# Kernel optimization log

Measured on AMD Instinct MI355X. Metric: run time of the kernel, lower is better.

The kernel has to match this reference:

```python
import jax, jax.numpy as jnp
import numpy as np

B, N, INPUT_DIM = 32, 4096, 256
BASE = 32           # base_feat_dim
A = 5               # n_aggs
E = 48              # per_agg_dim
H = 2               # num_agg_heads
HD = E // H         # head dim = 24
AGG_DIM = BASE * A  # 160
HIDDEN = 512
EXTRA_IN = INPUT_DIM - AGG_DIM   # 96
EXTRA_OUT = HIDDEN - E * A       # 272


def setup_inputs() -> dict:
    key = jax.random.key(0)
    ks = jax.random.split(key, 10)
    s = 0.05
    return {
        "x": jax.random.normal(ks[0], (B, N, INPUT_DIM), dtype=jnp.float32),
        # 5 per-group Linear(base_feat_dim -> 48), stacked: [A, E, BASE]
        "agg_W": jax.random.normal(ks[1], (A, E, BASE), dtype=jnp.float32) * s,
        "agg_b": jax.random.normal(ks[2], (A, E), dtype=jnp.float32) * s,
        # MultiheadAttention packed in-projection [3E, E] and bias [3E]
        "in_proj_w": jax.random.normal(ks[3], (3 * E, E), dtype=jnp.float32) * s,
        "in_proj_b": jax.random.normal(ks[4], (3 * E,), dtype=jnp.float32) * s,
        "out_w": jax.random.normal(ks[5], (E, E), dtype=jnp.float32) * s,
        "out_b": jax.random.normal(ks[6], (E,), dtype=jnp.float32) * s,
        # extra Linear(96 -> 272)
        "extra_w": jax.random.normal(ks[7], (EXTRA_OUT, EXTRA_IN), dtype=jnp.float32) * s,
        "extra_b": jax.random.normal(ks[8], (EXTRA_OUT,), dtype=jnp.float32) * s,
    }


def reference(x, agg_W, agg_b, in_proj_w, in_proj_b, out_w, out_b, extra_w, extra_b):
    b, n, _ = x.shape
    agg_feat = x[..., :AGG_DIM].reshape(b, n, A, BASE)      # [B,N,A,BASE]
    extra_feat = x[..., AGG_DIM:]                            # [B,N,EXTRA_IN]

    # fused per-group projections (one batched GEMM)
    proj = jnp.einsum("bnad,aed->bnae", agg_feat, agg_W) + agg_b  # [B,N,A,E]

    # faithful to torch: stack(dim=1) -> [B,A,N,E], then reshape(B*N, A, E)
    stacked = jnp.transpose(proj, (0, 2, 1, 3)).reshape(b * n, A, E)

    # MultiheadAttention (eval mode; attn dropout inactive)
    qkv = stacked @ in_proj_w.T + in_proj_b                  # [M,A,3E]
    q, k, v = jnp.split(qkv, 3, axis=-1)
    def heads(t):  # [M,A,E] -> [M,H,A,HD]
        return t.reshape(-1, A, H, HD).transpose(0, 2, 1, 3)
    q, k, v = heads(q), heads(k), heads(v)
    scores = jnp.einsum("mhqd,mhkd->mhqk", q, k) / np.sqrt(HD).astype(np.float32)
    attn = jax.nn.softmax(scores, axis=-1)
    o = jnp.einsum("mhqk,mhkd->mhqd", attn, v)               # [M,H,A,HD]
    o = o.transpose(0, 2, 1, 3).reshape(-1, A, E)            # [M,A,E]
    attn_out = o @ out_w.T + out_b

    agg_out = attn_out.reshape(b, n, A * E)                  # [B,N,240]
    extra_out = extra_feat @ extra_w.T + extra_b             # [B,N,272]
    return jnp.concatenate([agg_out, extra_out], axis=-1)    # [B,N,512]
```

## Files before the change

### kernel.cpp

```cpp
#include <hip/hip_runtime.h>

#define NTOK (32*4096)
#define WQ_FLOATS (5*144*32)

__global__ void setup_wqkv(const float* __restrict__ aggW,
                           const float* __restrict__ aggB,
                           const float* __restrict__ ipw,
                           const float* __restrict__ ipb,
                           float* __restrict__ Wq,
                           float* __restrict__ bq)
{
    int t = blockIdx.x*256 + threadIdx.x;
    if (t >= 5*144) return;
    int a = t / 144;
    int r = t - a*144;
    float scale = (r < 48) ? 0.20412414523193154f : 1.0f;
    const float* wrow = ipw + r*48;
    float bacc = ipb[r];
    for (int e = 0; e < 48; ++e) bacc += wrow[e]*aggB[a*48 + e];
    bq[t] = bacc*scale;
    for (int d = 0; d < 32; ++d) {
        float acc = 0.f;
        for (int e = 0; e < 48; ++e) acc += wrow[e]*aggW[(a*48 + e)*32 + d];
        Wq[t*32 + d] = acc*scale;
    }
}

__device__ __forceinline__ void load_xchunk(const float* __restrict__ p, float xr[32])
{
    const float4* xv = reinterpret_cast<const float4*>(p);
#pragma unroll
    for (int i = 0; i < 8; ++i) {
        float4 t = xv[i];
        xr[4*i+0] = t.x; xr[4*i+1] = t.y; xr[4*i+2] = t.z; xr[4*i+3] = t.w;
    }
}

__device__ __forceinline__ float row32(const float* __restrict__ wrow, const float xr[32], float acc)
{
    const float4* wp = reinterpret_cast<const float4*>(wrow);
#pragma unroll
    for (int i = 0; i < 8; ++i) {
        float4 w4 = wp[i];
        acc = fmaf(w4.x, xr[4*i+0], acc);
        acc = fmaf(w4.y, xr[4*i+1], acc);
        acc = fmaf(w4.z, xr[4*i+2], acc);
        acc = fmaf(w4.w, xr[4*i+3], acc);
    }
    return acc;
}

__global__ __launch_bounds__(256) void attn_main(
    const float* __restrict__ x,
    const float* __restrict__ Wq,
    const float* __restrict__ bq,
    const float* __restrict__ outw,
    const float* __restrict__ outb,
    float* __restrict__ out)
{
    __shared__ float sAll[11856];
    float* sW   = sAll;
    float* sB   = sAll + 9216;
    float* sOWT = sAll + 9504;
    float* sOB  = sAll + 11808;

    const int t = (int)threadIdx.x;
    const unsigned g0 = blockIdx.x * 240u;
    const unsigned u0 = g0 >> 12;
    const unsigned a0 = u0 - 5u*((u0*52429u) >> 18);
    const unsigned a1 = (a0 == 4u) ? 0u : a0 + 1u;

    {
        const float4* s0p = reinterpret_cast<const float4*>(Wq + a0*4608u);
        const float4* s1p = reinterpret_cast<const float4*>(Wq + a1*4608u);
        float4* d0 = reinterpret_cast<float4*>(sW);
        float4* d1 = reinterpret_cast<float4*>(sW + 4608);
#pragma unroll
        for (int i = 0; i < 5; ++i) {
            int idx = t + 256*i;
            if (idx < 1152) { d0[idx] = s0p[idx]; d1[idx] = s1p[idx]; }
        }
#pragma unroll
        for (int i = 0; i < 9; ++i) {
            int idx = t + 256*i;
            int f = idx / 48, j = idx - f*48;
            sOWT[idx] = outw[j*48 + f];
        }
        if (t < 144) { sB[t] = bq[a0*144u + t]; sB[144 + t] = bq[a1*144u + t]; }
        if (t >= 192 && t < 240) sOB[t - 192] = outb[t - 192];
    }
    __syncthreads();

    const int lane = t & 63;
    if (lane >= 60) return;
    const int wv = t >> 6;
    const unsigned m_base = (blockIdx.x*4u + (unsigned)wv)*12u;
    const unsigned tok5 = (unsigned)lane / 5u;
    const unsigned aq   = (unsigned)lane - tok5*5u;
    const unsigned m = m_base + tok5;
    if (m >= NTOK) return;

    const unsigned g  = 5u*m_base + (unsigned)lane;
    const unsigned u  = g >> 12;
    const unsigned bb = (u*52429u) >> 18;
    const unsigned a  = u - 5u*bb;
    const float* xp = x + ((((bb<<12) | (g & 4095u)) << 8) + (a<<5));

    const int sel = (a == a0) ? 0 : 1;
    const float* myW = sW + sel*4608;
    const float* myB = sB + sel*144;

    float xr[32]; load_xchunk(xp, xr);

    const int base4 = (lane - (int)aq)*4;
    int ad[4];
#pragma unroll
    for (int r = 0; r < 4; ++r) {
        int sl = (int)aq + r + 1; if (sl >= 5) sl -= 5;
        ad[r] = base4 + sl*4;
    }

    float s0[5] = {0,0,0,0,0}, s1[5] = {0,0,0,0,0};
#pragma unroll 1
    for (int e = 0; e < 24; ++e) {
        float qe = row32(myW + e*32, xr, myB[e]);
        float ke = row32(myW + (48+e)*32, xr, myB[48+e]);
        s0[0] = fmaf(qe, ke, s0[0]);
#pragma unroll
        for (int r = 0; r < 4; ++r) {
            float kr = __int_as_float(__builtin_amdgcn_ds_bpermute(ad[r], __float_as_int(ke)));
            s0[r+1] = fmaf(qe, kr, s0[r+1]);
        }
    }
#pragma unroll 1
    for (int e = 24; e < 48; ++e) {
        float qe = row32(myW + e*32, xr, myB[e]);
        float ke = row32(myW + (48+e)*32, xr, myB[48+e]);
        s1[0] = fmaf(qe, ke, s1[0]);
#pragma unroll
        for (int r = 0; r < 4; ++r) {
            float kr = __int_as_float(__builtin_amdgcn_ds_bpermute(ad[r], __float_as_int(ke)));
            s1[r+1] = fmaf(qe, kr, s1[r+1]);
        }
    }

    float p0[5], p1[5];
    {
        float mx = fmaxf(fmaxf(fmaxf(s0[0], s0[1]), fmaxf(s0[2], s0[3])), s0[4]);
        float e0 = __expf(s0[0]-mx), e1 = __expf(s0[1]-mx), e2 = __expf(s0[2]-mx),
              e3 = __expf(s0[3]-mx), e4 = __expf(s0[4]-mx);
        float inv = 1.0f/(e0+e1+e2+e3+e4);
        p0[0]=e0*inv; p0[1]=e1*inv; p0[2]=e2*inv; p0[3]=e3*inv; p0[4]=e4*inv;
    }
    {
        float mx = fmaxf(fmaxf(fmaxf(s1[0], s1[1]), fmaxf(s1[2], s1[3])), s1[4]);
        float e0 = __expf(s1[0]-mx), e1 = __expf(s1[1]-mx), e2 = __expf(s1[2]-mx),
              e3 = __expf(s1[3]-mx), e4 = __expf(s1[4]-mx);
        float inv = 1.0f/(e0+e1+e2+e3+e4);
        p1[0]=e0*inv; p1[1]=e1*inv; p1[2]=e2*inv; p1[3]=e3*inv; p1[4]=e4*inv;
    }

    float oj[48];
    {
        const float4* b4 = reinterpret_cast<const float4*>(sOB);
#pragma unroll
        for (int j4 = 0; j4 < 12; ++j4) {
            float4 v = b4[j4];
            oj[4*j4+0]=v.x; oj[4*j4+1]=v.y; oj[4*j4+2]=v.z; oj[4*j4+3]=v.w;
        }
    }
#pragma unroll 1
    for (int e = 0; e < 24; ++e) {
        float ve = row32(myW + (96+e)*32, xr, myB[96+e]);
        float oe = p0[0]*ve;
#pragma unroll
        for (int r = 0; r < 4; ++r) {
            float vr = __int_as_float(__builtin_amdgcn_ds_bpermute(ad[r], __float_as_int(ve)));
            oe = fmaf(p0[r+1], vr, oe);
        }
        const float4* owr = reinterpret_cast<const float4*>(sOWT + e*48);
#pragma unroll
        for (int j4 = 0; j4 < 12; ++j4) {
            float4 w4 = owr[j4];
            oj[4*j4+0] = fmaf(w4.x, oe, oj[4*j4+0]);
            oj[4*j4+1] = fmaf(w4.y, oe, oj[4*j4+1]);
            oj[4*j4+2] = fmaf(w4.z, oe, oj[4*j4+2]);
            oj[4*j4+3] = fmaf(w4.w, oe, oj[4*j4+3]);
        }
    }
#pragma unroll 1
    for (int e = 24; e < 48; ++e) {
        float ve = row32(myW + (96+e)*32, xr, myB[96+e]);
        float oe = p1[0]*ve;
#pragma unroll
        for (int r = 0; r < 4; ++r) {
            float vr = __int_as_float(__builtin_amdgcn_ds_bpermute(ad[r], __float_as_int(ve)));
            oe = fmaf(p1[r+1], vr, oe);
        }
        const float4* owr = reinterpret_cast<const float4*>(sOWT + e*48);
#pragma unroll
        for (int j4 = 0; j4 < 12; ++j4) {
            float4 w4 = owr[j4];
            oj[4*j4+0] = fmaf(w4.x, oe, oj[4*j4+0]);
            oj[4*j4+1] = fmaf(w4.y, oe, oj[4*j4+1]);
            oj[4*j4+2] = fmaf(w4.z, oe, oj[4*j4+2]);
            oj[4*j4+3] = fmaf(w4.w, oe, oj[4*j4+3]);
        }
    }

    float4* d4 = reinterpret_cast<float4*>(out + (size_t)m*512u + aq*48u);
#pragma unroll
    for (int j4 = 0; j4 < 12; ++j4)
        d4[j4] = make_float4(oj[4*j4+0], oj[4*j4+1], oj[4*j4+2], oj[4*j4+3]);
}

__global__ __launch_bounds__(256) void extra_gemm(
    const float* __restrict__ x,
    const float* __restrict__ exw,
    const float* __restrict__ exb,
    float* __restrict__ out)
{
    __shared__ float sx[64*97];
    __shared__ float sw[16*292];

    const int t = (int)threadIdx.x;
    const unsigned m0 = blockIdx.x*64u;

#pragma unroll
    for (int i = 0; i < 6; ++i) {
        int idx = t + 256*i;
        int row = idx / 24, c4 = idx - row*24;
        float4 v = *reinterpret_cast<const float4*>(
            x + (size_t)(m0 + (unsigned)row)*256u + 160u + (unsigned)(c4*4));
        float* dp = sx + row*97 + c4*4;
        dp[0]=v.x; dp[1]=v.y; dp[2]=v.z; dp[3]=v.w;
    }

    const int ty = t >> 4;
    const int tx = t & 15;

    float acc[4][18];
#pragma unroll
    for (int i = 0; i < 4; ++i)
#pragma unroll
        for (int j = 0; j < 18; ++j) acc[i][j] = 0.f;

#pragma unroll 1
    for (int kp = 0; kp < 6; ++kp) {
        __syncthreads();
        {
            const float* gp = exw + (size_t)t*96u + (unsigned)(kp*16);
#pragma unroll
            for (int k4 = 0; k4 < 4; ++k4) {
                float4 v = *reinterpret_cast<const float4*>(gp + k4*4);
                sw[(k4*4+0)*292 + t] = v.x;
                sw[(k4*4+1)*292 + t] = v.y;
                sw[(k4*4+2)*292 + t] = v.z;
                sw[(k4*4+3)*292 + t] = v.w;
            }
            if (t < 32) {
                int col = 256 + t;
                if (col < 272) {
                    const float* gp2 = exw + (size_t)col*96u + (unsigned)(kp*16);
#pragma unroll
                    for (int k4 = 0; k4 < 4; ++k4) {
                        float4 v = *reinterpret_cast<const float4*>(gp2 + k4*4);
                        sw[(k4*4+0)*292 + col] = v.x;
                        sw[(k4*4+1)*292 + col] = v.y;
                        sw[(k4*4+2)*292 + col] = v.z;
                        sw[(k4*4+3)*292 + col] = v.w;
                    }
                } else {
#pragma unroll
                    for (int k = 0; k < 16; ++k) sw[k*292 + col] = 0.f;
                }
            }
        }
        __syncthreads();

#pragma unroll
        for (int kk = 0; kk < 16; ++kk) {
            float xv[4];
#pragma unroll
            for (int i = 0; i < 4; ++i)
                xv[i] = sx[(ty*4 + i)*97 + kp*16 + kk];
            const float* wrow = sw + kk*292 + tx*18;
            float wv[18];
#pragma unroll
            for (int j2 = 0; j2 < 9; ++j2) {
                float2 w2 = *reinterpret_cast<const float2*>(wrow + j2*2);
                wv[2*j2] = w2.x; wv[2*j2+1] = w2.y;
            }
#pragma unroll
            for (int i = 0; i < 4; ++i)
#pragma unroll
                for (int j = 0; j < 18; ++j)
                    acc[i][j] = fmaf(xv[i], wv[j], acc[i][j]);
        }
    }

#pragma unroll
    for (int i = 0; i < 4; ++i) {
        size_t ob = (size_t)(m0 + (unsigned)(ty*4 + i))*512u + 240u;
#pragma unroll
        for (int j = 0; j < 18; ++j) {
            int col = tx*18 + j;
            if (col < 272) out[ob + col] = acc[i][j] + exb[col];
        }
    }
}

extern "C" void kernel_launch(void* const* d_in, const int* in_sizes, int n_in,
                              void* d_out, int out_size, void* d_ws, size_t ws_size,
                              hipStream_t stream)
{
    const float* x    = (const float*)d_in[0];
    const float* aggW = (const float*)d_in[1];
    const float* aggB = (const float*)d_in[2];
    const float* ipw  = (const float*)d_in[3];
    const float* ipb  = (const float*)d_in[4];
    const float* outw = (const float*)d_in[5];
    const float* outb = (const float*)d_in[6];
    const float* exw  = (const float*)d_in[7];
    const float* exb  = (const float*)d_in[8];
    float* out = (float*)d_out;

    float* Wq = (float*)d_ws;
    float* bq = Wq + WQ_FLOATS;

    setup_wqkv<<<dim3(3), dim3(256), 0, stream>>>(aggW, aggB, ipw, ipb, Wq, bq);
    attn_main<<<dim3((NTOK + 47)/48), dim3(256), 0, stream>>>(x, Wq, bq, outw, outb, out);
    extra_gemm<<<dim3(NTOK/64), dim3(256), 0, stream>>>(x, exw, exb, out);
}
```

Before: 822.7 us.

## Restructure extra GEMM to one-token-per-thread with shared weight broadcast; split row32 accumulators

The extra linear kernel now gives each thread one token with its 96 inputs held in registers. Each block stages half of the weight matrix (136 columns) in shared memory, interleaved so that a wave reads it as broadcast float4 loads, and writes float4 outputs directly. This removes the per-k-tile syncs and the 2D register tiling. In exchange each token row of x is read by two blocks and register pressure is high (96 floats). Separately, row32 splits its dot product into four partial accumulators to shorten the FMA dependency chain.

```diff
diff --git a/kernel.cpp b/kernel.cpp
--- a/kernel.cpp
+++ b/kernel.cpp
@@ -36,18 +36,35 @@
     }
 }
 
-__device__ __forceinline__ float row32(const float* __restrict__ wrow, const float xr[32], float acc)
+__device__ __forceinline__ float row32(const float* __restrict__ wrow, const float xr[32], float bias)
 {
     const float4* wp = reinterpret_cast<const float4*>(wrow);
-#pragma unroll
-    for (int i = 0; i < 8; ++i) {
+    float a0 = bias, a1 = 0.f, a2 = 0.f, a3 = 0.f;
+#pragma unroll
+    for (int i = 0; i < 2; ++i) {
         float4 w4 = wp[i];
-        acc = fmaf(w4.x, xr[4*i+0], acc);
-        acc = fmaf(w4.y, xr[4*i+1], acc);
-        acc = fmaf(w4.z, xr[4*i+2], acc);
-        acc = fmaf(w4.w, xr[4*i+3], acc);
-    }
-    return acc;
+        a0 = fmaf(w4.x, xr[4*i+0], a0); a0 = fmaf(w4.y, xr[4*i+1], a0);
+        a0 = fmaf(w4.z, xr[4*i+2], a0); a0 = fmaf(w4.w, xr[4*i+3], a0);
+    }
+#pragma unroll
+    for (int i = 2; i < 4; ++i) {
+        float4 w4 = wp[i];
+        a1 = fmaf(w4.x, xr[4*i+0], a1); a1 = fmaf(w4.y, xr[4*i+1], a1);
+        a1 = fmaf(w4.z, xr[4*i+2], a1); a1 = fmaf(w4.w, xr[4*i+3], a1);
+    }
+#pragma unroll
+    for (int i = 4; i < 6; ++i) {
+        float4 w4 = wp[i];
+        a2 = fmaf(w4.x, xr[4*i+0], a2); a2 = fmaf(w4.y, xr[4*i+1], a2);
+        a2 = fmaf(w4.z, xr[4*i+2], a2); a2 = fmaf(w4.w, xr[4*i+3], a2);
+    }
+#pragma unroll
+    for (int i = 6; i < 8; ++i) {
+        float4 w4 = wp[i];
+        a3 = fmaf(w4.x, xr[4*i+0], a3); a3 = fmaf(w4.y, xr[4*i+1], a3);
+        a3 = fmaf(w4.z, xr[4*i+2], a3); a3 = fmaf(w4.w, xr[4*i+3], a3);
+    }
+    return (a0 + a1) + (a2 + a3);
 }
 
 __global__ __launch_bounds__(256) void attn_main(
@@ -220,93 +237,51 @@
     const float* __restrict__ exb,
     float* __restrict__ out)
 {
-    __shared__ float sx[64*97];
-    __shared__ float sw[16*292];
+    __shared__ float sw[34*96*4];
 
     const int t = (int)threadIdx.x;
-    const unsigned m0 = blockIdx.x*64u;
-
-#pragma unroll
-    for (int i = 0; i < 6; ++i) {
-        int idx = t + 256*i;
-        int row = idx / 24, c4 = idx - row*24;
+    const unsigned tb = blockIdx.x >> 1;
+    const int half = (int)(blockIdx.x & 1u);
+    const int colbase = half*136;
+
+#pragma unroll 1
+    for (int q = t; q < 3264; q += 256) {
+        int row = q / 24;
+        int kp  = (q - row*24)*4;
         float4 v = *reinterpret_cast<const float4*>(
-            x + (size_t)(m0 + (unsigned)row)*256u + 160u + (unsigned)(c4*4));
-        float* dp = sx + row*97 + c4*4;
-        dp[0]=v.x; dp[1]=v.y; dp[2]=v.z; dp[3]=v.w;
-    }
-
-    const int ty = t >> 4;
-    const int tx = t & 15;
-
-    float acc[4][18];
-#pragma unroll
-    for (int i = 0; i < 4; ++i)
-#pragma unroll
-        for (int j = 0; j < 18; ++j) acc[i][j] = 0.f;
-
-#pragma unroll 1
-    for (int kp = 0; kp < 6; ++kp) {
-        __syncthreads();
-        {
-            const float* gp = exw + (size_t)t*96u + (unsigned)(kp*16);
-#pragma unroll
-            for (int k4 = 0; k4 < 4; ++k4) {
-                float4 v = *reinterpret_cast<const float4*>(gp + k4*4);
-                sw[(k4*4+0)*292 + t] = v.x;
-                sw[(k4*4+1)*292 + t] = v.y;
-                sw[(k4*4+2)*292 + t] = v.z;
-                sw[(k4*4+3)*292 + t] = v.w;
-            }
-            if (t < 32) {
-                int col = 256 + t;
-                if (col < 272) {
-                    const float* gp2 = exw + (size_t)col*96u + (unsigned)(kp*16);
-#pragma unroll
-                    for (int k4 = 0; k4 < 4; ++k4) {
-                        float4 v = *reinterpret_cast<const float4*>(gp2 + k4*4);
-                        sw[(k4*4+0)*292 + col] = v.x;
-                        sw[(k4*4+1)*292 + col] = v.y;
-                        sw[(k4*4+2)*292 + col] = v.z;
-                        sw[(k4*4+3)*292 + col] = v.w;
-                    }
-                } else {
-#pragma unroll
-                    for (int k = 0; k < 16; ++k) sw[k*292 + col] = 0.f;
-                }
-            }
-        }
-        __syncthreads();
-
-#pragma unroll
-        for (int kk = 0; kk < 16; ++kk) {
-            float xv[4];
-#pragma unroll
-            for (int i = 0; i < 4; ++i)
-                xv[i] = sx[(ty*4 + i)*97 + kp*16 + kk];
-            const float* wrow = sw + kk*292 + tx*18;
-            float wv[18];
-#pragma unroll
-            for (int j2 = 0; j2 < 9; ++j2) {
-                float2 w2 = *reinterpret_cast<const float2*>(wrow + j2*2);
-                wv[2*j2] = w2.x; wv[2*j2+1] = w2.y;
-            }
-#pragma unroll
-            for (int i = 0; i < 4; ++i)
-#pragma unroll
-                for (int j = 0; j < 18; ++j)
-                    acc[i][j] = fmaf(xv[i], wv[j], acc[i][j]);
-        }
-    }
-
-#pragma unroll
-    for (int i = 0; i < 4; ++i) {
-        size_t ob = (size_t)(m0 + (unsigned)(ty*4 + i))*512u + 240u;
-#pragma unroll
-        for (int j = 0; j < 18; ++j) {
-            int col = tx*18 + j;
-            if (col < 272) out[ob + col] = acc[i][j] + exb[col];
-        }
+            exw + (size_t)(colbase + row)*96u + (unsigned)kp);
+        int c4 = row >> 2, jp = row & 3;
+        float* dp = sw + (c4*96 + kp)*4 + jp;
+        dp[0] = v.x; dp[4] = v.y; dp[8] = v.z; dp[12] = v.w;
+    }
+
+    const unsigned m = tb*256u + (unsigned)t;
+    float xr[96];
+    {
+        const float4* xp = reinterpret_cast<const float4*>(x + (size_t)m*256u + 160u);
+#pragma unroll
+        for (int i = 0; i < 24; ++i) {
+            float4 v = xp[i];
+            xr[4*i+0]=v.x; xr[4*i+1]=v.y; xr[4*i+2]=v.z; xr[4*i+3]=v.w;
+        }
+    }
+    __syncthreads();
+
+    float* __restrict__ dst = out + (size_t)m*512u + 240u + (unsigned)colbase;
+    const float4* bp = reinterpret_cast<const float4*>(exb + colbase);
+#pragma unroll 1
+    for (int c4 = 0; c4 < 34; ++c4) {
+        const float4* wp = reinterpret_cast<const float4*>(sw + c4*384);
+        float4 acc = bp[c4];
+#pragma unroll
+        for (int k = 0; k < 96; ++k) {
+            float4 w4 = wp[k];
+            acc.x = fmaf(w4.x, xr[k], acc.x);
+            acc.y = fmaf(w4.y, xr[k], acc.y);
+            acc.z = fmaf(w4.z, xr[k], acc.z);
+            acc.w = fmaf(w4.w, xr[k], acc.w);
+        }
+        reinterpret_cast<float4*>(dst)[c4] = acc;
     }
 }
 
@@ -330,5 +305,5 @@
 
     setup_wqkv<<<dim3(3), dim3(256), 0, stream>>>(aggW, aggB, ipw, ipb, Wq, bq);
     attn_main<<<dim3((NTOK + 47)/48), dim3(256), 0, stream>>>(x, Wq, bq, outw, outb, out);
-    extra_gemm<<<dim3(NTOK/64), dim3(256), 0, stream>>>(x, exw, exb, out);
-}
+    extra_gemm<<<dim3(512*2), dim3(256), 0, stream>>>(x, exw, exb, out);
+}
```

Result: faster. 741.2 us (-9.9%).
